# Kernel tuning notes

Hardware: AMD Instinct MI355X
Metric: run time of the kernel (lower is better)

The kernel has to match this reference:

```python
import jax, jax.numpy as jnp
import numpy as np

B, S, E, H = 4, 8192, 1024, 16
D = E // H  # head_dim = 64


def setup_inputs() -> dict:
    key = jax.random.key(0)
    ks = jax.random.split(key, 9)
    s = 0.02
    return {
        "x": jax.random.normal(ks[0], (B, S, E), dtype=jnp.float32),
        "Wq": jax.random.normal(ks[1], (D, E), dtype=jnp.float32) * s,
        "bq": jax.random.normal(ks[2], (D,), dtype=jnp.float32) * s,
        "Wk": jax.random.normal(ks[3], (D, E), dtype=jnp.float32) * s,
        "bk": jax.random.normal(ks[4], (D,), dtype=jnp.float32) * s,
        "Wv": jax.random.normal(ks[5], (D, E), dtype=jnp.float32) * s,
        "bv": jax.random.normal(ks[6], (D,), dtype=jnp.float32) * s,
        "Wo": jax.random.normal(ks[7], (E, E), dtype=jnp.float32) * s,
        "bo": jax.random.normal(ks[8], (E,), dtype=jnp.float32) * s,
    }


def reference(x, Wq, bq, Wk, bk, Wv, bv, Wo, bo):
    b, s, e = x.shape
    d = Wq.shape[0]          # head_dim (projections map embed_dim -> head_dim)
    h = e // d               # num_heads
    # torch Linear: y = x @ W.T + b ; projected shape [B, S, d]
    # view(B, -1, h, d) on [B, S, d] => effective seq S' = S // h (faithful to source)
    def split_heads(t):
        return t.reshape(b, -1, h, d).transpose(0, 2, 1, 3)  # [B, H, S', D]
    q = split_heads(x @ Wq.T + bq)
    k = split_heads(x @ Wk.T + bk)
    v = split_heads(x @ Wv.T + bv)
    scores = jnp.einsum('bhqd,bhkd->bhqk', q, k) / np.sqrt(d).astype(jnp.float32)
    attn = jax.nn.softmax(scores, axis=-1)  # dropout=0.0 => identity
    ctx = jnp.einsum('bhqk,bhkd->bhqd', attn, v)
    ctx = ctx.transpose(0, 2, 1, 3).reshape(b, -1, e)  # [B, S', E]
    return ctx @ Wo.T + bo
```

## Files before the change

### kernel.cpp

```cpp
#include <hip/hip_runtime.h>
#include <hip/hip_bf16.h>


typedef unsigned short u16;
typedef __attribute__((ext_vector_type(8))) short short8;
typedef __attribute__((ext_vector_type(4))) float f32x4;

#define VMWAIT(N) asm volatile("s_waitcnt vmcnt(" #N ")" ::: "memory")
#define MEMFENCE() asm volatile("" ::: "memory")
#define BAR() __builtin_amdgcn_s_barrier()

__device__ inline u16 f2bf(float f) {
    union { float f; unsigned u; } v; v.f = f;
    unsigned u = v.u;
    return (u16)((u + 0x7fffu + ((u >> 16) & 1u)) >> 16);
}
__device__ inline unsigned pack_bf2(float a, float b) {
    union { __hip_bfloat162 h; unsigned u; } v;
    v.h = __float22bfloat162_rn(float2{a, b});
    return v.u;
}
__device__ __forceinline__ void gld16(void* lds, const void* gptr) {
    __builtin_amdgcn_global_load_lds(
        (const __attribute__((address_space(1))) unsigned int*)gptr,
        (__attribute__((address_space(3))) unsigned int*)lds,
        16, 0, 0);
}

__global__ __launch_bounds__(256) void convw(
    const float* __restrict__ Wq, const float* __restrict__ bq,
    const float* __restrict__ Wk, const float* __restrict__ bk,
    const float* __restrict__ Wv, const float* __restrict__ bv,
    const float* __restrict__ Wo,
    u16* __restrict__ Wqkv, float* __restrict__ qkvb, u16* __restrict__ Wob)
{
    const int idx = blockIdx.x * 256 + threadIdx.x;
    Wob[idx] = f2bf(Wo[idx]);
    if (idx < 196608) {
        const int row = idx >> 10, k = idx & 1023;
        float v = (row < 64)  ? Wq[row * 1024 + k] * 0.125f
                : (row < 128) ? Wk[(row - 64) * 1024 + k]
                              : Wv[(row - 128) * 1024 + k];
        Wqkv[idx] = f2bf(v);
    }
    if (idx < 192) {
        qkvb[idx] = (idx < 64) ? bq[idx] * 0.125f
                  : (idx < 128) ? bk[idx - 64] : bv[idx - 128];
    }
}

__global__ __launch_bounds__(512, 4) void qkv_gemm(
    const float* __restrict__ X, const u16* __restrict__ W,
    const float* __restrict__ bias, u16* __restrict__ Out)
{
    __shared__ short8 Bs[3][1536];

    const int tid = threadIdx.x;
    const int lane = tid & 63, wid = tid >> 6;
    const int q = lane >> 4, r = lane & 15;
    const int wm = wid >> 1, wn = wid & 1;
    const long m0 = (long)blockIdx.x * 64;

    const u16* wp[3];
    #pragma unroll
    for (int i = 0; i < 3; ++i) {
        const int p = wid * 3 + i, kk2 = p / 12, nt = p % 12;
        wp[i] = W + (long)(nt * 16 + r) * 1024 + kk2 * 32 + q * 8;
    }

    const float* px = X + (m0 + wm * 16 + r) * 1024 + q * 8;

    f32x4 acc[6] = {};
    float4 a[3][4];

#define LOADA(s, j) do {                                            \
        a[s][0] = *(const float4*)(px + (j) * 64);                  \
        a[s][1] = *(const float4*)(px + (j) * 64 + 4);              \
        a[s][2] = *(const float4*)(px + (j) * 64 + 32);             \
        a[s][3] = *(const float4*)(px + (j) * 64 + 36);             \
    } while (0)

#define STAGE(j) do {                                               \
        _Pragma("unroll")                                           \
        for (int i = 0; i < 3; ++i)                                 \
            gld16(&Bs[(j) % 3][(wid * 3 + i) * 64], wp[i] + (j) * 64); \
    } while (0)

    LOADA(0, 0);  MEMFENCE();
    STAGE(0);     MEMFENCE();
    LOADA(1, 1);  MEMFENCE();
    STAGE(1);     MEMFENCE();
    LOADA(2, 2);  MEMFENCE();

    #pragma unroll
    for (int k = 0; k < 16; ++k) {
        const int slot = k % 3;
        if (k + 2 < 16) { STAGE(k + 2); MEMFENCE(); }
        if (k < 14)       VMWAIT(14);
        else if (k == 14) VMWAIT(7);
        else              VMWAIT(0);
        BAR();
        MEMFENCE();
        #pragma unroll
        for (int kk2 = 0; kk2 < 2; ++kk2) {
            union { short8 s; unsigned u[4]; } af;
            af.u[0] = pack_bf2(a[slot][kk2 * 2].x, a[slot][kk2 * 2].y);
            af.u[1] = pack_bf2(a[slot][kk2 * 2].z, a[slot][kk2 * 2].w);
            af.u[2] = pack_bf2(a[slot][kk2 * 2 + 1].x, a[slot][kk2 * 2 + 1].y);
            af.u[3] = pack_bf2(a[slot][kk2 * 2 + 1].z, a[slot][kk2 * 2 + 1].w);
            #pragma unroll
            for (int j = 0; j < 6; ++j) {
                const short8 bf = Bs[slot][(kk2 * 12 + wn * 6 + j) * 64 + lane];
                acc[j] = __builtin_amdgcn_mfma_f32_16x16x32_bf16(
                    af.s, bf, acc[j], 0, 0, 0);
            }
        }
        MEMFENCE();
        if (k + 3 < 16) { LOADA(slot, k + 3); MEMFENCE(); }
        BAR();
    }
#undef LOADA
#undef STAGE

    u16* lds0 = (u16*)&Bs[0][0];
    #pragma unroll
    for (int j = 0; j < 6; ++j) {
        const int col = wn * 96 + j * 16 + r;
        const float badd = bias[col];
        #pragma unroll
        for (int e = 0; e < 4; ++e)
            lds0[(wm * 16 + q * 4 + e) * 192 + col] = f2bf(acc[j][e] + badd);
    }
    asm volatile("s_waitcnt lgkmcnt(0)" ::: "memory");
    BAR();
    const short8* l8 = (const short8*)lds0;
    u16* ob = Out + m0 * 192;
    #pragma unroll
    for (int s = 0; s < 3; ++s) {
        short8 v = l8[tid + s * 512];
        *(short8*)(ob + (long)(tid + s * 512) * 8) = v;
    }
}

__global__ __launch_bounds__(256) void vtrans(
    const u16* __restrict__ qkv, u16* __restrict__ Vt)
{
    __shared__ u16 T[64][68];
    const int bh = blockIdx.x, b = bh >> 4, h = bh & 15;
    const int i0 = blockIdx.y * 64;
    const int tid = threadIdx.x;

    #pragma unroll
    for (int it = 0; it < 2; ++it) {
        const int c = tid + 256 * it;
        const int il = c >> 3, d8 = (c & 7) * 8;
        short8 v = *(const short8*)(qkv +
            ((long)b * 8192 + (long)(i0 + il) * 16 + h) * 192 + 128 + d8);
        #pragma unroll
        for (int j = 0; j < 8; ++j) T[d8 + j][il] = (u16)v[j];
    }
    __syncthreads();
    #pragma unroll
    for (int it = 0; it < 2; ++it) {
        const int c = tid + 256 * it;
        const int dl = c >> 3, i8 = (c & 7) * 8;
        short8 o;
        #pragma unroll
        for (int j = 0; j < 8; ++j) o[j] = (short)T[dl][i8 + j];
        *(short8*)(Vt + ((long)bh * 64 + dl) * 512 + i0 + i8) = o;
    }
}

__global__ __launch_bounds__(256) void attn_flash(
    const u16* __restrict__ qkv, const u16* __restrict__ Vt,
    u16* __restrict__ ctx)
{
    __shared__ short8 Ks[2][512];
    __shared__ short8 Vs[2][512];
    __shared__ u16 Plds[4][16 * 72];

    const int tid = threadIdx.x, lane = tid & 63, wid = tid >> 6;
    const int q = lane >> 4, r = lane & 15;
    const int qt = blockIdx.x;
    const int bh = blockIdx.y;
    const int b = bh >> 4, h = bh & 15;
    const long qrowbase = (long)b * 8192 + h;

    short8 Qf0, Qf1;
    {
        const int i = qt * 64 + wid * 16 + r;
        const u16* p = qkv + (qrowbase + (long)i * 16) * 192 + q * 8;
        Qf0 = *(const short8*)(p);
        Qf1 = *(const short8*)(p + 32);
    }

    const u16* kbase = qkv + (qrowbase + (long)(wid * 16 + r) * 16) * 192
                           + 64 + q * 8;
    const u16* vbase = Vt + ((long)bh * 64 + wid * 16 + r) * 512 + q * 8;

    gld16(&Ks[0][wid * 64],       kbase);
    gld16(&Ks[0][256 + wid * 64], kbase + 32);
    gld16(&Vs[0][wid * 64],       vbase);
    gld16(&Vs[0][256 + wid * 64], vbase + 32);

    f32x4 O[4] = {};
    float mrun = -1e30f, lrun = 0.f;
    u16* Pw = &Plds[wid][0];

    for (int c = 0; c < 8; ++c) {
        const int j0 = c * 64, buf = c & 1;
        if (c < 7) {
            const u16* kp = kbase + (long)(j0 + 64) * 3072;
            const u16* vp = vbase + j0 + 64;
            gld16(&Ks[buf ^ 1][wid * 64],       kp);
            gld16(&Ks[buf ^ 1][256 + wid * 64], kp + 32);
            gld16(&Vs[buf ^ 1][wid * 64],       vp);
            gld16(&Vs[buf ^ 1][256 + wid * 64], vp + 32);
            VMWAIT(4);
        } else {
            VMWAIT(0);
        }
        BAR();
        MEMFENCE();
        f32x4 S[4];
        #pragma unroll
        for (int ct = 0; ct < 4; ++ct) {
            f32x4 s = {};
            s = __builtin_amdgcn_mfma_f32_16x16x32_bf16(
                Ks[buf][ct * 64 + lane], Qf0, s, 0, 0, 0);
            s = __builtin_amdgcn_mfma_f32_16x16x32_bf16(
                Ks[buf][256 + ct * 64 + lane], Qf1, s, 0, 0, 0);
            S[ct] = s;
        }
        float mc = -1e30f;
        #pragma unroll
        for (int ct = 0; ct < 4; ++ct)
            mc = fmaxf(mc, fmaxf(fmaxf(S[ct][0], S[ct][1]),
                                 fmaxf(S[ct][2], S[ct][3])));
        mc = fmaxf(mc, __shfl_xor(mc, 16, 64));
        mc = fmaxf(mc, __shfl_xor(mc, 32, 64));
        const float mnew = fmaxf(mrun, mc);
        const float alpha = __expf(mrun - mnew);
        mrun = mnew;
        float se = 0.f;
        #pragma unroll
        for (int ct = 0; ct < 4; ++ct)
            #pragma unroll
            for (int e = 0; e < 4; ++e) {
                const float pv = __expf(S[ct][e] - mnew);
                S[ct][e] = pv; se += pv;
            }
        se += __shfl_xor(se, 16, 64);
        se += __shfl_xor(se, 32, 64);
        lrun = lrun * alpha + se;
        #pragma unroll
        for (int nt = 0; nt < 4; ++nt)
            #pragma unroll
            for (int e = 0; e < 4; ++e) O[nt][e] *= alpha;
        #pragma unroll
        for (int ct = 0; ct < 4; ++ct) {
            uint2 d;
            d.x = pack_bf2(S[ct][0], S[ct][1]);
            d.y = pack_bf2(S[ct][2], S[ct][3]);
            *(uint2*)(Pw + r * 72 + ct * 16 + q * 4) = d;
        }
        short8 Pf0 = *(const short8*)(Pw + r * 72 + q * 8);
        short8 Pf1 = *(const short8*)(Pw + r * 72 + 32 + q * 8);
        #pragma unroll
        for (int nt = 0; nt < 4; ++nt) {
            O[nt] = __builtin_amdgcn_mfma_f32_16x16x32_bf16(
                Vs[buf][nt * 64 + lane], Pf0, O[nt], 0, 0, 0);
            O[nt] = __builtin_amdgcn_mfma_f32_16x16x32_bf16(
                Vs[buf][256 + nt * 64 + lane], Pf1, O[nt], 0, 0, 0);
        }
        MEMFENCE();
        BAR();
    }

    const float inv = 1.0f / lrun;
    const long i = qt * 64 + wid * 16 + r;
    u16* po = ctx + ((long)b * 512 + i) * 1024 + h * 64;
    #pragma unroll
    for (int nt = 0; nt < 4; ++nt) {
        uint2 d;
        d.x = pack_bf2(O[nt][0] * inv, O[nt][1] * inv);
        d.y = pack_bf2(O[nt][2] * inv, O[nt][3] * inv);
        *(uint2*)(po + nt * 16 + q * 4) = d;
    }
}

__global__ __launch_bounds__(256) void gemm_o(
    const u16* __restrict__ A, const u16* __restrict__ B,
    const float* __restrict__ bias, float* __restrict__ C)
{
    __shared__ short8 As[2][512];
    __shared__ short8 Bs[2][512];

    const int tid = threadIdx.x;
    const int lane = tid & 63, wid = tid >> 6;
    const int q = lane >> 4, r = lane & 15;
    const long m0 = (long)blockIdx.x * 64, n0 = (long)blockIdx.y * 64;
    const int wm = wid >> 1, wn = wid & 1;

    const u16* ap[2];
    const u16* bp[2];
    #pragma unroll
    for (int i = 0; i < 2; ++i) {
        const int t = wid * 2 + i, f = t >> 2, mt = t & 3;
        ap[i] = A + (m0 + mt * 16 + r) * 1024 + f * 32 + q * 8;
        bp[i] = B + (n0 + mt * 16 + r) * 1024 + f * 32 + q * 8;
    }

    #pragma unroll
    for (int i = 0; i < 2; ++i) {
        gld16(&As[0][(wid * 2 + i) * 64], ap[i]);
        gld16(&Bs[0][(wid * 2 + i) * 64], bp[i]);
    }

    f32x4 acc[2][2] = {};

    for (int k0 = 0; k0 < 1024; k0 += 64) {
        const int buf = (k0 >> 6) & 1;
        if (k0 + 64 < 1024) {
            #pragma unroll
            for (int i = 0; i < 2; ++i) {
                gld16(&As[buf ^ 1][(wid * 2 + i) * 64], ap[i] + k0 + 64);
                gld16(&Bs[buf ^ 1][(wid * 2 + i) * 64], bp[i] + k0 + 64);
            }
            VMWAIT(4);
        } else {
            VMWAIT(0);
        }
        BAR();
        MEMFENCE();
        #pragma unroll
        for (int f = 0; f < 2; ++f) {
            short8 af0 = As[buf][f * 256 + (wm * 2 + 0) * 64 + lane];
            short8 af1 = As[buf][f * 256 + (wm * 2 + 1) * 64 + lane];
            short8 bf0 = Bs[buf][f * 256 + (wn * 2 + 0) * 64 + lane];
            short8 bf1 = Bs[buf][f * 256 + (wn * 2 + 1) * 64 + lane];
            acc[0][0] = __builtin_amdgcn_mfma_f32_16x16x32_bf16(af0, bf0, acc[0][0], 0, 0, 0);
            acc[0][1] = __builtin_amdgcn_mfma_f32_16x16x32_bf16(af0, bf1, acc[0][1], 0, 0, 0);
            acc[1][0] = __builtin_amdgcn_mfma_f32_16x16x32_bf16(af1, bf0, acc[1][0], 0, 0, 0);
            acc[1][1] = __builtin_amdgcn_mfma_f32_16x16x32_bf16(af1, bf1, acc[1][1], 0, 0, 0);
        }
        MEMFENCE();
        BAR();
    }

    #pragma unroll
    for (int i = 0; i < 2; ++i)
        #pragma unroll
        for (int j = 0; j < 2; ++j) {
            const long col = n0 + (wn * 2 + j) * 16 + r;
            const float badd = bias[col];
            #pragma unroll
            for (int e = 0; e < 4; ++e) {
                const long row = m0 + (wm * 2 + i) * 16 + q * 4 + e;
                C[row * 1024 + col] = acc[i][j][e] + badd;
            }
        }
}

extern "C" void kernel_launch(void* const* d_in, const int* in_sizes, int n_in,
                              void* d_out, int out_size, void* d_ws, size_t ws_size,
                              hipStream_t stream)
{
    const float* x  = (const float*)d_in[0];
    const float* Wq = (const float*)d_in[1];
    const float* bq = (const float*)d_in[2];
    const float* Wk = (const float*)d_in[3];
    const float* bk = (const float*)d_in[4];
    const float* Wv = (const float*)d_in[5];
    const float* bv = (const float*)d_in[6];
    const float* Wo = (const float*)d_in[7];
    const float* bo = (const float*)d_in[8];
    float* out = (float*)d_out;
    char* ws = (char*)d_ws;

    u16*   qkv  = (u16*)(ws);
    u16*   Vt   = (u16*)(ws + 12582912);
    u16*   Wqkv = (u16*)(ws + 16777216);
    u16*   Wob  = (u16*)(ws + 17170432);
    float* qkvb = (float*)(ws + 19267584);
    u16*   ctx  = (u16*)(ws + 19268352);

    convw<<<4096, 256, 0, stream>>>(Wq, bq, Wk, bk, Wv, bv, Wo, Wqkv, qkvb, Wob);
    qkv_gemm<<<512, 512, 0, stream>>>(x, Wqkv, qkvb, qkv);
    vtrans<<<dim3(64, 8), 256, 0, stream>>>(qkv, Vt);
    attn_flash<<<dim3(8, 64), 256, 0, stream>>>(qkv, Vt, ctx);
    gemm_o<<<dim3(32, 16), 256, 0, stream>>>(ctx, Wob, bo, out);
}
```

Baseline: 263.1 us.

## Stage X tiles through swizzled LDS and double the QKV GEMM row tile

```diff
diff --git a/kernel.cpp b/kernel.cpp
--- a/kernel.cpp
+++ b/kernel.cpp
@@ -49,17 +49,18 @@
     }
 }
 
-__global__ __launch_bounds__(512, 4) void qkv_gemm(
+__global__ __launch_bounds__(512) void qkv_gemm(
     const float* __restrict__ X, const u16* __restrict__ W,
     const float* __restrict__ bias, u16* __restrict__ Out)
 {
-    __shared__ short8 Bs[3][1536];
+    __shared__ float  Xs[2][8192];
+    __shared__ short8 Ws[2][1536];
 
     const int tid = threadIdx.x;
     const int lane = tid & 63, wid = tid >> 6;
     const int q = lane >> 4, r = lane & 15;
     const int wm = wid >> 1, wn = wid & 1;
-    const long m0 = (long)blockIdx.x * 64;
+    const long m0 = (long)blockIdx.x * 128;
 
     const u16* wp[3];
     #pragma unroll
@@ -68,75 +69,94 @@
         wp[i] = W + (long)(nt * 16 + r) * 1024 + kk2 * 32 + q * 8;
     }
 
-    const float* px = X + (m0 + wm * 16 + r) * 1024 + q * 8;
-
-    f32x4 acc[6] = {};
-    float4 a[3][4];
-
-#define LOADA(s, j) do {                                            \
-        a[s][0] = *(const float4*)(px + (j) * 64);                  \
-        a[s][1] = *(const float4*)(px + (j) * 64 + 4);              \
-        a[s][2] = *(const float4*)(px + (j) * 64 + 32);             \
-        a[s][3] = *(const float4*)(px + (j) * 64 + 36);             \
+    const float* pxa[4];
+    #pragma unroll
+    for (int i = 0; i < 4; ++i) {
+        const int s = i * 512 + wid * 64 + lane;
+        const int row = s >> 4;
+        const int c = (s & 15) ^ (row & 7);
+        pxa[i] = X + (m0 + row) * 1024 + c * 4;
+    }
+
+#define STAGEA(b, k) do {                                              \
+        _Pragma("unroll")                                              \
+        for (int i = 0; i < 4; ++i)                                    \
+            gld16(&Xs[b][(i * 512 + wid * 64) * 4], pxa[i] + (k) * 64); \
     } while (0)
 
-#define STAGE(j) do {                                               \
-        _Pragma("unroll")                                           \
-        for (int i = 0; i < 3; ++i)                                 \
-            gld16(&Bs[(j) % 3][(wid * 3 + i) * 64], wp[i] + (j) * 64); \
+#define STAGEW(b, k) do {                                              \
+        _Pragma("unroll")                                              \
+        for (int i = 0; i < 3; ++i)                                    \
+            gld16(&Ws[b][(wid * 3 + i) * 64], wp[i] + (k) * 64);       \
     } while (0)
 
-    LOADA(0, 0);  MEMFENCE();
-    STAGE(0);     MEMFENCE();
-    LOADA(1, 1);  MEMFENCE();
-    STAGE(1);     MEMFENCE();
-    LOADA(2, 2);  MEMFENCE();
-
-    #pragma unroll
+    f32x4 acc[2][6] = {};
+
+    STAGEA(0, 0);
+    STAGEW(0, 0);
+    MEMFENCE();
+
     for (int k = 0; k < 16; ++k) {
-        const int slot = k % 3;
-        if (k + 2 < 16) { STAGE(k + 2); MEMFENCE(); }
-        if (k < 14)       VMWAIT(14);
-        else if (k == 14) VMWAIT(7);
-        else              VMWAIT(0);
+        const int buf = k & 1;
+        if (k < 15) {
+            STAGEA(buf ^ 1, k + 1);
+            STAGEW(buf ^ 1, k + 1);
+            MEMFENCE();
+            VMWAIT(7);
+        } else {
+            VMWAIT(0);
+        }
         BAR();
         MEMFENCE();
         #pragma unroll
         for (int kk2 = 0; kk2 < 2; ++kk2) {
-            union { short8 s; unsigned u[4]; } af;
-            af.u[0] = pack_bf2(a[slot][kk2 * 2].x, a[slot][kk2 * 2].y);
-            af.u[1] = pack_bf2(a[slot][kk2 * 2].z, a[slot][kk2 * 2].w);
-            af.u[2] = pack_bf2(a[slot][kk2 * 2 + 1].x, a[slot][kk2 * 2 + 1].y);
-            af.u[3] = pack_bf2(a[slot][kk2 * 2 + 1].z, a[slot][kk2 * 2 + 1].w);
+            union { short8 s; unsigned u[4]; } af[2];
+            #pragma unroll
+            for (int mt = 0; mt < 2; ++mt) {
+                const int row = wm * 32 + mt * 16 + r;
+                const int c0 = kk2 * 8 + q * 2;
+                const float4 f0 = *(const float4*)
+                    &Xs[buf][row * 64 + ((c0    ) ^ (row & 7)) * 4];
+                const float4 f1 = *(const float4*)
+                    &Xs[buf][row * 64 + ((c0 + 1) ^ (row & 7)) * 4];
+                af[mt].u[0] = pack_bf2(f0.x, f0.y);
+                af[mt].u[1] = pack_bf2(f0.z, f0.w);
+                af[mt].u[2] = pack_bf2(f1.x, f1.y);
+                af[mt].u[3] = pack_bf2(f1.z, f1.w);
+            }
             #pragma unroll
             for (int j = 0; j < 6; ++j) {
-                const short8 bf = Bs[slot][(kk2 * 12 + wn * 6 + j) * 64 + lane];
-                acc[j] = __builtin_amdgcn_mfma_f32_16x16x32_bf16(
-                    af.s, bf, acc[j], 0, 0, 0);
+                const short8 bf = Ws[buf][(kk2 * 12 + wn * 6 + j) * 64 + lane];
+                acc[0][j] = __builtin_amdgcn_mfma_f32_16x16x32_bf16(
+                    af[0].s, bf, acc[0][j], 0, 0, 0);
+                acc[1][j] = __builtin_amdgcn_mfma_f32_16x16x32_bf16(
+                    af[1].s, bf, acc[1][j], 0, 0, 0);
             }
         }
         MEMFENCE();
-        if (k + 3 < 16) { LOADA(slot, k + 3); MEMFENCE(); }
-        BAR();
-    }
-#undef LOADA
-#undef STAGE
-
-    u16* lds0 = (u16*)&Bs[0][0];
+        BAR();
+    }
+#undef STAGEA
+#undef STAGEW
+
+    u16* lds0 = (u16*)&Xs[0][0];
     #pragma unroll
     for (int j = 0; j < 6; ++j) {
         const int col = wn * 96 + j * 16 + r;
         const float badd = bias[col];
         #pragma unroll
-        for (int e = 0; e < 4; ++e)
-            lds0[(wm * 16 + q * 4 + e) * 192 + col] = f2bf(acc[j][e] + badd);
+        for (int mt = 0; mt < 2; ++mt)
+            #pragma unroll
+            for (int e = 0; e < 4; ++e)
+                lds0[(wm * 32 + mt * 16 + q * 4 + e) * 192 + col] =
+                    f2bf(acc[mt][j][e] + badd);
     }
     asm volatile("s_waitcnt lgkmcnt(0)" ::: "memory");
     BAR();
     const short8* l8 = (const short8*)lds0;
     u16* ob = Out + m0 * 192;
     #pragma unroll
-    for (int s = 0; s < 3; ++s) {
+    for (int s = 0; s < 6; ++s) {
         short8 v = l8[tid + s * 512];
         *(short8*)(ob + (long)(tid + s * 512) * 8) = v;
     }
@@ -386,7 +406,7 @@
     u16*   ctx  = (u16*)(ws + 19268352);
 
     convw<<<4096, 256, 0, stream>>>(Wq, bq, Wk, bk, Wv, bv, Wo, Wqkv, qkvb, Wob);
-    qkv_gemm<<<512, 512, 0, stream>>>(x, Wqkv, qkvb, qkv);
+    qkv_gemm<<<256, 512, 0, stream>>>(x, Wqkv, qkvb, qkv);
     vtrans<<<dim3(64, 8), 256, 0, stream>>>(qkv, Vt);
     attn_flash<<<dim3(8, 64), 256, 0, stream>>>(qkv, Vt, ctx);
     gemm_o<<<dim3(32, 16), 256, 0, stream>>>(ctx, Wob, bo, out);
```

After: 262.6 us. About the same (-0.2%).
